# Kernel tuning notes

Measured on AMD Instinct MI355X. Metric: run time of the kernel, lower is better.

The kernel has to match this reference:

```python
import jax, jax.numpy as jnp
import numpy as np

H = 3  # hidden_size


def _gru_layer(x_seq, h0, W_ih, W_hh, b_ih, b_hh):
    # x_seq: [B, T, I]; W_ih: [3H, I]; W_hh: [3H, H]; gate order (PyTorch): r, z, n
    xW = jnp.einsum('bti,gi->btg', x_seq, W_ih) + b_ih  # [B, T, 3H], precomputed once

    def step(h, xw_t):
        gh = h @ W_hh.T + b_hh                      # [B, 3H]
        xr, xz, xn = jnp.split(xw_t, 3, axis=-1)
        hr, hz, hn = jnp.split(gh, 3, axis=-1)
        r = jax.nn.sigmoid(xr + hr)
        z = jax.nn.sigmoid(xz + hz)
        n = jnp.tanh(xn + r * hn)
        h_new = (1.0 - z) * n + z * h
        return h_new, h_new

    h_last, hs = jax.lax.scan(step, h0, jnp.swapaxes(xW, 0, 1))  # scan over T
    return h_last, jnp.swapaxes(hs, 0, 1)  # [B,H], [B,T,H]


def setup_inputs() -> dict:
    key = jax.random.key(0)
    ks = jax.random.split(key, 9)
    B, T, I = 2048, 512, 64
    s0 = 1.0 / np.sqrt(H)
    inp = {
        'x': jax.random.normal(ks[0], (B, T, I), dtype=jnp.float32),
        # layer 0: input I -> hidden H
        'W_ih0': jax.random.uniform(ks[1], (3 * H, I), jnp.float32, -s0, s0),
        'W_hh0': jax.random.uniform(ks[2], (3 * H, H), jnp.float32, -s0, s0),
        'b_ih0': jax.random.uniform(ks[3], (3 * H,), jnp.float32, -s0, s0),
        'b_hh0': jax.random.uniform(ks[4], (3 * H,), jnp.float32, -s0, s0),
        # layer 1: hidden H -> hidden H
        'W_ih1': jax.random.uniform(ks[5], (3 * H, H), jnp.float32, -s0, s0),
        'W_hh1': jax.random.uniform(ks[6], (3 * H, H), jnp.float32, -s0, s0),
        'b_ih1': jax.random.uniform(ks[7], (3 * H,), jnp.float32, -s0, s0),
        'b_hh1': jax.random.uniform(ks[8], (3 * H,), jnp.float32, -s0, s0),
    }
    return inp


def reference(x, W_ih0, W_hh0, b_ih0, b_hh0, W_ih1, W_hh1, b_ih1, b_hh1):
    B = x.shape[0]
    h0 = jnp.zeros((B, H), dtype=x.dtype)
    # layer 0
    _, seq0 = _gru_layer(x, h0, W_ih0, W_hh0, b_ih0, b_hh0)
    # layer 1; module returns h_out[-1] = final hidden state of the last layer
    h_last, _ = _gru_layer(seq0, h0, W_ih1, W_hh1, b_ih1, b_hh1)
    return h_last  # [B, H]
```

## Files before the change

### kernel.cpp

```cpp
#include <hip/hip_runtime.h>

#define BB 2048
#define TT 512
#define II 64
#define XWS 12

#define LOG2E 1.44269504088896340736f

__device__ __forceinline__ float fexp2(float x) {
#if __has_builtin(__builtin_amdgcn_exp2f)
    return __builtin_amdgcn_exp2f(x);
#else
    return __expf(x * 0.69314718055994531f);
#endif
}
__device__ __forceinline__ float frcp(float x) {
#if __has_builtin(__builtin_amdgcn_rcpf)
    return __builtin_amdgcn_rcpf(x);
#else
    return __fdividef(1.f, x);
#endif
}

#define QB0(v) __int_as_float(__builtin_amdgcn_mov_dpp(__float_as_int(v), 0x00, 0xF, 0xF, 1))
#define QB1(v) __int_as_float(__builtin_amdgcn_mov_dpp(__float_as_int(v), 0x55, 0xF, 0xF, 1))
#define QB2(v) __int_as_float(__builtin_amdgcn_mov_dpp(__float_as_int(v), 0xAA, 0xF, 0xF, 1))

__global__ __launch_bounds__(256) void xw_kernel(
    const float* __restrict__ x, const float* __restrict__ W_ih0,
    const float* __restrict__ b_ih0, float* __restrict__ xw)
{
    __shared__ float wt[II * XWS];
    __shared__ float bias[XWS];
    const int tid = threadIdx.x;

    for (int idx = tid; idx < 9 * II; idx += 256) {
        int i = idx & 63, g = idx >> 6;
        int c = g / 3, j = g - c * 3;
        float sc = (c == 2) ? (2.0f * LOG2E) : (-LOG2E);
        wt[i * XWS + j * 4 + c] = W_ih0[idx] * sc;
    }
    if (tid < XWS) {
        int j = tid >> 2, c = tid & 3;
        float v = 0.f;
        if (c < 3) {
            float sc = (c == 2) ? (2.0f * LOG2E) : (-LOG2E);
            v = b_ih0[c * 3 + j] * sc;
        }
        bias[tid] = v;
    }
    __syncthreads();

    const int R = blockIdx.x * 256 + tid;
    const float* xr = x + (size_t)R * II;

    float a[XWS];
#pragma unroll
    for (int u = 0; u < XWS; ++u) a[u] = bias[u];

#pragma unroll
    for (int i0 = 0; i0 < II; i0 += 4) {
        float4 xv = *(const float4*)(xr + i0);
        float xs[4] = {xv.x, xv.y, xv.z, xv.w};
#pragma unroll
        for (int d = 0; d < 4; ++d) {
            const float4* w4 = (const float4*)&wt[(i0 + d) * XWS];
            float4 w0 = w4[0], w1 = w4[1], w2 = w4[2];
            float v = xs[d];
            a[0] = fmaf(v, w0.x, a[0]);
            a[1] = fmaf(v, w0.y, a[1]);
            a[2] = fmaf(v, w0.z, a[2]);
            a[4] = fmaf(v, w1.x, a[4]);
            a[5] = fmaf(v, w1.y, a[5]);
            a[6] = fmaf(v, w1.z, a[6]);
            a[8] = fmaf(v, w2.x, a[8]);
            a[9] = fmaf(v, w2.y, a[9]);
            a[10] = fmaf(v, w2.z, a[10]);
        }
    }

    float* o = xw + (size_t)R * XWS;
    *(float4*)(o + 0) = make_float4(a[0], a[1], a[2], 0.f);
    *(float4*)(o + 4) = make_float4(a[4], a[5], a[6], 0.f);
    *(float4*)(o + 8) = make_float4(a[8], a[9], a[10], 0.f);
}

__global__ __launch_bounds__(512) void gru_rec(
    const float* __restrict__ xw,
    const float* __restrict__ W_hh0, const float* __restrict__ b_hh0,
    const float* __restrict__ W_ih1, const float* __restrict__ b_ih1,
    const float* __restrict__ W_hh1, const float* __restrict__ b_hh1,
    float* __restrict__ out)
{
    const int tid = threadIdx.x;
    const int j   = tid & 3;
    const int jj  = (j < 3) ? j : 2;
    const int s   = (blockIdx.x * 512 + tid) >> 2;

    float wh0[3][3], wi1[3][3], wh1[3][3], bh0[3], bi1[3], bh1[3];
#pragma unroll
    for (int c = 0; c < 3; ++c) {
        float sc = (c == 2) ? (2.0f * LOG2E) : (-LOG2E);
        int row = c * 3 + jj;
#pragma unroll
        for (int k = 0; k < 3; ++k) {
            wh0[c][k] = W_hh0[row * 3 + k] * sc;
            wi1[c][k] = W_ih1[row * 3 + k] * sc;
            wh1[c][k] = W_hh1[row * 3 + k] * sc;
        }
        bh0[c] = b_hh0[row] * sc;
        bi1[c] = b_ih1[row] * sc;
        bh1[c] = b_hh1[row] * sc;
    }

    float h00 = 0.f, h01 = 0.f, h02 = 0.f;
    float h10 = 0.f, h11 = 0.f, h12 = 0.f;
    float h0j = 0.f, h1j = 0.f;

    const float* base = xw + ((size_t)s * TT) * XWS + jj * 4;

    auto LD = [&](int t) -> float4 {
        t = (t < TT) ? t : (TT - 1);
        return *(const float4*)(base + (size_t)t * XWS);
    };

    auto STEP = [&](float4 xq) {
        float hr = fmaf(wh0[0][2], h02, fmaf(wh0[0][1], h01, fmaf(wh0[0][0], h00, bh0[0])));
        float hz = fmaf(wh0[1][2], h02, fmaf(wh0[1][1], h01, fmaf(wh0[1][0], h00, bh0[1])));
        float hn = fmaf(wh0[2][2], h02, fmaf(wh0[2][1], h01, fmaf(wh0[2][0], h00, bh0[2])));
        float r = frcp(1.f + fexp2(xq.x + hr));
        float z = frcp(1.f + fexp2(xq.y + hz));
        float q = fmaf(r, hn, xq.z);
        float n = fmaf(-2.f, frcp(1.f + fexp2(q)), 1.f);
        h0j = fmaf(z, h0j - n, n);
        h00 = QB0(h0j); h01 = QB1(h0j); h02 = QB2(h0j);
        float a0 = fmaf(wi1[0][2], h02, fmaf(wi1[0][1], h01, fmaf(wi1[0][0], h00, bi1[0])));
        float a1 = fmaf(wi1[1][2], h02, fmaf(wi1[1][1], h01, fmaf(wi1[1][0], h00, bi1[1])));
        float a2 = fmaf(wi1[2][2], h02, fmaf(wi1[2][1], h01, fmaf(wi1[2][0], h00, bi1[2])));
        float g0 = fmaf(wh1[0][2], h12, fmaf(wh1[0][1], h11, fmaf(wh1[0][0], h10, bh1[0])));
        float g1 = fmaf(wh1[1][2], h12, fmaf(wh1[1][1], h11, fmaf(wh1[1][0], h10, bh1[1])));
        float g2 = fmaf(wh1[2][2], h12, fmaf(wh1[2][1], h11, fmaf(wh1[2][0], h10, bh1[2])));
        float r1 = frcp(1.f + fexp2(a0 + g0));
        float z1 = frcp(1.f + fexp2(a1 + g1));
        float q1 = fmaf(r1, g2, a2);
        float n1 = fmaf(-2.f, frcp(1.f + fexp2(q1)), 1.f);
        h1j = fmaf(z1, h1j - n1, n1);
        h10 = QB0(h1j); h11 = QB1(h1j); h12 = QB2(h1j);
    };

    float4 P0 = LD(0), P1 = LD(1), P2 = LD(2), P3 = LD(3);
    for (int t = 0; t < TT; t += 4) {
        float4 N0 = LD(t + 4), N1 = LD(t + 5), N2 = LD(t + 6), N3 = LD(t + 7);
        STEP(P0); STEP(P1); STEP(P2); STEP(P3);
        P0 = N0; P1 = N1; P2 = N2; P3 = N3;
    }

    if (j < 3) out[s * 3 + j] = h1j;
}

extern "C" void kernel_launch(void* const* d_in, const int* in_sizes, int n_in,
                              void* d_out, int out_size, void* d_ws, size_t ws_size,
                              hipStream_t stream) {
    const float* x     = (const float*)d_in[0];
    const float* W_ih0 = (const float*)d_in[1];
    const float* W_hh0 = (const float*)d_in[2];
    const float* b_ih0 = (const float*)d_in[3];
    const float* b_hh0 = (const float*)d_in[4];
    const float* W_ih1 = (const float*)d_in[5];
    const float* W_hh1 = (const float*)d_in[6];
    const float* b_ih1 = (const float*)d_in[7];
    const float* b_hh1 = (const float*)d_in[8];
    float* out = (float*)d_out;
    float* xw  = (float*)d_ws;

    hipLaunchKernelGGL(xw_kernel, dim3((BB * TT) / 256), dim3(256), 0, stream,
                       x, W_ih0, b_ih0, xw);
    hipLaunchKernelGGL(gru_rec, dim3((BB * 4) / 512), dim3(512), 0, stream,
                       xw, W_hh0, b_hh0, W_ih1, b_ih1, W_hh1, b_hh1, out);
}
```

Baseline: 649.9 us.

## Spread GRU recurrence over single-wave blocks, deepen prefetch, multi-row xw kernel

The recurrent kernel now launches 64-thread, single-wavefront blocks, giving 128 blocks instead of 16 blocks of eight waves. This spreads the latency-bound serial chains over many more CUs and SIMDs. The xw loads are now issued as a rolling 8-deep prefetch interleaved with the steps, to hide global-memory latency better. The input projection kernel computes four rows per thread, so each LDS weight read is reused four times, at the cost of more registers per thread.

```diff
diff --git a/kernel.cpp b/kernel.cpp
--- a/kernel.cpp
+++ b/kernel.cpp
@@ -26,7 +26,7 @@
 #define QB1(v) __int_as_float(__builtin_amdgcn_mov_dpp(__float_as_int(v), 0x55, 0xF, 0xF, 1))
 #define QB2(v) __int_as_float(__builtin_amdgcn_mov_dpp(__float_as_int(v), 0xAA, 0xF, 0xF, 1))
 
-__global__ __launch_bounds__(256) void xw_kernel(
+__global__ __launch_bounds__(256, 4) void xw_kernel(
     const float* __restrict__ x, const float* __restrict__ W_ih0,
     const float* __restrict__ b_ih0, float* __restrict__ xw)
 {
@@ -51,41 +51,57 @@
     }
     __syncthreads();
 
-    const int R = blockIdx.x * 256 + tid;
-    const float* xr = x + (size_t)R * II;
-
-    float a[XWS];
-#pragma unroll
-    for (int u = 0; u < XWS; ++u) a[u] = bias[u];
+    const int R0 = blockIdx.x * 1024 + tid;
+    const float* xr = x + (size_t)R0 * II;
+
+    float a[4][XWS];
+    {
+        float bb[XWS];
+#pragma unroll
+        for (int u = 0; u < XWS; ++u) bb[u] = bias[u];
+#pragma unroll
+        for (int r = 0; r < 4; ++r)
+#pragma unroll
+            for (int u = 0; u < XWS; ++u) a[r][u] = bb[u];
+    }
 
 #pragma unroll
     for (int i0 = 0; i0 < II; i0 += 4) {
-        float4 xv = *(const float4*)(xr + i0);
-        float xs[4] = {xv.x, xv.y, xv.z, xv.w};
+        float4 xv[4];
+#pragma unroll
+        for (int r = 0; r < 4; ++r)
+            xv[r] = *(const float4*)(xr + (size_t)r * 256 * II + i0);
 #pragma unroll
         for (int d = 0; d < 4; ++d) {
             const float4* w4 = (const float4*)&wt[(i0 + d) * XWS];
             float4 w0 = w4[0], w1 = w4[1], w2 = w4[2];
-            float v = xs[d];
-            a[0] = fmaf(v, w0.x, a[0]);
-            a[1] = fmaf(v, w0.y, a[1]);
-            a[2] = fmaf(v, w0.z, a[2]);
-            a[4] = fmaf(v, w1.x, a[4]);
-            a[5] = fmaf(v, w1.y, a[5]);
-            a[6] = fmaf(v, w1.z, a[6]);
-            a[8] = fmaf(v, w2.x, a[8]);
-            a[9] = fmaf(v, w2.y, a[9]);
-            a[10] = fmaf(v, w2.z, a[10]);
+#pragma unroll
+            for (int r = 0; r < 4; ++r) {
+                float v = (d == 0) ? xv[r].x : (d == 1) ? xv[r].y
+                        : (d == 2) ? xv[r].z : xv[r].w;
+                a[r][0]  = fmaf(v, w0.x, a[r][0]);
+                a[r][1]  = fmaf(v, w0.y, a[r][1]);
+                a[r][2]  = fmaf(v, w0.z, a[r][2]);
+                a[r][4]  = fmaf(v, w1.x, a[r][4]);
+                a[r][5]  = fmaf(v, w1.y, a[r][5]);
+                a[r][6]  = fmaf(v, w1.z, a[r][6]);
+                a[r][8]  = fmaf(v, w2.x, a[r][8]);
+                a[r][9]  = fmaf(v, w2.y, a[r][9]);
+                a[r][10] = fmaf(v, w2.z, a[r][10]);
+            }
         }
     }
 
-    float* o = xw + (size_t)R * XWS;
-    *(float4*)(o + 0) = make_float4(a[0], a[1], a[2], 0.f);
-    *(float4*)(o + 4) = make_float4(a[4], a[5], a[6], 0.f);
-    *(float4*)(o + 8) = make_float4(a[8], a[9], a[10], 0.f);
-}
-
-__global__ __launch_bounds__(512) void gru_rec(
+#pragma unroll
+    for (int r = 0; r < 4; ++r) {
+        float* o = xw + ((size_t)R0 + r * 256) * XWS;
+        *(float4*)(o + 0) = make_float4(a[r][0], a[r][1], a[r][2], 0.f);
+        *(float4*)(o + 4) = make_float4(a[r][4], a[r][5], a[r][6], 0.f);
+        *(float4*)(o + 8) = make_float4(a[r][8], a[r][9], a[r][10], 0.f);
+    }
+}
+
+__global__ __launch_bounds__(64, 1) void gru_rec(
     const float* __restrict__ xw,
     const float* __restrict__ W_hh0, const float* __restrict__ b_hh0,
     const float* __restrict__ W_ih1, const float* __restrict__ b_ih1,
@@ -95,7 +111,7 @@
     const int tid = threadIdx.x;
     const int j   = tid & 3;
     const int jj  = (j < 3) ? j : 2;
-    const int s   = (blockIdx.x * 512 + tid) >> 2;
+    const int s   = (blockIdx.x * 64 + tid) >> 2;
 
     float wh0[3][3], wi1[3][3], wh1[3][3], bh0[3], bi1[3], bh1[3];
 #pragma unroll
@@ -148,11 +164,18 @@
         h10 = QB0(h1j); h11 = QB1(h1j); h12 = QB2(h1j);
     };
 
-    float4 P0 = LD(0), P1 = LD(1), P2 = LD(2), P3 = LD(3);
-    for (int t = 0; t < TT; t += 4) {
-        float4 N0 = LD(t + 4), N1 = LD(t + 5), N2 = LD(t + 6), N3 = LD(t + 7);
-        STEP(P0); STEP(P1); STEP(P2); STEP(P3);
-        P0 = N0; P1 = N1; P2 = N2; P3 = N3;
+    float4 R0 = LD(0), R1 = LD(1), R2 = LD(2), R3 = LD(3),
+           R4 = LD(4), R5 = LD(5), R6 = LD(6), R7 = LD(7);
+
+    for (int t = 0; t < TT; t += 8) {
+        STEP(R0); R0 = LD(t + 8);
+        STEP(R1); R1 = LD(t + 9);
+        STEP(R2); R2 = LD(t + 10);
+        STEP(R3); R3 = LD(t + 11);
+        STEP(R4); R4 = LD(t + 12);
+        STEP(R5); R5 = LD(t + 13);
+        STEP(R6); R6 = LD(t + 14);
+        STEP(R7); R7 = LD(t + 15);
     }
 
     if (j < 3) out[s * 3 + j] = h1j;
@@ -173,8 +196,8 @@
     float* out = (float*)d_out;
     float* xw  = (float*)d_ws;
 
-    hipLaunchKernelGGL(xw_kernel, dim3((BB * TT) / 256), dim3(256), 0, stream,
+    hipLaunchKernelGGL(xw_kernel, dim3((BB * TT) / 1024), dim3(256), 0, stream,
                        x, W_ih0, b_ih0, xw);
-    hipLaunchKernelGGL(gru_rec, dim3((BB * 4) / 512), dim3(512), 0, stream,
+    hipLaunchKernelGGL(gru_rec, dim3((BB * 4) / 64), dim3(64), 0, stream,
                        xw, W_hh0, b_hh0, W_ih1, b_ih1, W_hh1, b_hh1, out);
 }
```

Result: slower. 917.1 us (+41.1%).
